# Kernel optimization log

Hardware: AMD Instinct MI355X
Metric: run time of the kernel (lower is better)

The kernel has to match this reference:

```python
import jax, jax.numpy as jnp
import numpy as np


def conv1d(x, w, b, pad):
    # x: [B, C, T], w: [O, I, K], b: [O]
    y = jax.lax.conv_general_dilated(x, w, (1,), [(pad, pad)],
                                     dimension_numbers=('NCH', 'OIH', 'NCH'))
    return y + b[None, :, None]


def chan_ln(x, g, b, eps=1e-4):
    # channel LayerNorm on [B, C, T] (normalize over C)
    mu = jnp.mean(x, axis=1, keepdims=True)
    var = jnp.mean((x - mu) ** 2, axis=1, keepdims=True)
    return (x - mu) * jax.lax.rsqrt(var + eps) * g[None, :, None] + b[None, :, None]


def setup_inputs() -> dict:
    key = jax.random.key(0)
    ks = jax.random.split(key, 16)
    B, Tph, Tmel, H, W = 8, 512, 4096, 256, 256
    x = jax.random.normal(ks[0], (B, Tph, H), jnp.float32)
    x_mask = jnp.ones((B, Tph, 1), jnp.float32)
    x2word = jnp.sort(jax.random.randint(ks[1], (B, Tph), 1, W + 1), axis=1)
    mel2word = jnp.sort(jax.random.randint(ks[2], (B, Tmel), 1, W + 1), axis=1)
    s = 0.05
    pre_w1 = jax.random.normal(ks[3], (H, H, 5), jnp.float32) * s
    pre_b1 = jnp.zeros((H,), jnp.float32)
    ln1_g = jnp.ones((H,), jnp.float32)
    ln1_b = jnp.zeros((H,), jnp.float32)
    pre_w2 = jax.random.normal(ks[4], (H, H, 5), jnp.float32) * s
    pre_b2 = jnp.zeros((H,), jnp.float32)
    ln2_g = jnp.ones((H,), jnp.float32)
    ln2_b = jnp.zeros((H,), jnp.float32)
    proj_w = jax.random.normal(ks[5], (H, H, 1), jnp.float32) * s
    proj_b = jnp.zeros((H,), jnp.float32)
    gauss_w = jax.random.normal(ks[6], (2, H, 1), jnp.float32) * s
    gauss_b = jnp.zeros((2,), jnp.float32)
    return {'x': x, 'x_mask': x_mask,
            'pre_w1': pre_w1, 'pre_b1': pre_b1, 'ln1_g': ln1_g, 'ln1_b': ln1_b,
            'pre_w2': pre_w2, 'pre_b2': pre_b2, 'ln2_g': ln2_g, 'ln2_b': ln2_b,
            'proj_w': proj_w, 'proj_b': proj_b,
            'gauss_w': gauss_w, 'gauss_b': gauss_b,
            'x2word': x2word, 'mel2word': mel2word, 'word_len': 256}


def reference(x, x_mask, pre_w1, pre_b1, ln1_g, ln1_b, pre_w2, pre_b2,
              ln2_g, ln2_b, proj_w, proj_b, gauss_w, gauss_b,
              x2word, mel2word, word_len):
    res_x = x                                   # [B, Tph, H]
    xt = jnp.swapaxes(x, 1, 2)                  # [B, H, Tph]
    mt = jnp.swapaxes(x_mask, 1, 2)             # [B, 1, Tph]
    # ConvReluNorm pre-net (dropout p=0)
    h = jax.nn.relu(chan_ln(conv1d(xt * mt, pre_w1, pre_b1, 2), ln1_g, ln1_b))
    h = jax.nn.relu(chan_ln(conv1d(h * mt, pre_w2, pre_b2, 2), ln2_g, ln2_b))
    h = (xt + conv1d(h, proj_w, proj_b, 0)) * mt
    # gaussian head -> per-phone duration mean m
    g = conv1d(h, gauss_w, gauss_b, 0)          # [B, 2, Tph]
    m = (jax.nn.relu(g[:, 0:1]) + 1.0) * mt
    m = m[:, 0, :]                              # [B, Tph]
    B, Tph = x2word.shape
    Tmel = mel2word.shape[1]
    W = word_len
    bidx = jnp.arange(B)[:, None]
    # scatter-add per-phone durations into word slots (slot 0 = pad)
    dur = jnp.zeros((B, W + 1), m.dtype).at[bidx, x2word].add(m)
    m_word = dur[:, 1:]                         # [B, W]
    # mel2ph_to_dur: frame counts per word
    dur_word = jnp.zeros((B, W + 1), m.dtype).at[bidx, mel2word].add(
        jnp.ones(mel2word.shape, m.dtype))[:, 1:]
    scale = dur_word / (m_word + 1e-4)
    scale_ph = jnp.pad(scale, ((0, 0), (1, 0)))[bidx, x2word]   # gather to phones
    m = m + (scale_ph - 1.0) * jax.lax.stop_gradient(m)
    # Gaussian soft alignment
    center = jnp.cumsum(m, axis=1) - m / 2                      # [B, Tph]
    pos = jnp.arange(Tmel, dtype=m.dtype)
    diff = center[:, None, :] - pos[None, :, None]              # [B, Tmel, Tph]
    y_mask = (mel2word > 0).astype(m.dtype)[:, :, None]
    yx = (mel2word[:, :, None] == x2word[:, None, :]).astype(m.dtype)
    yx = yx * y_mask * mt                                       # [B, Tmel, Tph]
    logits = -(diff * diff) / 10.0
    masked = logits - (1.0 - yx) * 1e9
    weights = jax.nn.softmax(masked.astype(jnp.float32), axis=2)
    attn = jnp.einsum('bmp,bph->bmh', weights, res_x)           # [B, Tmel, H]
    return attn, weights, m_word
```

## Files before the change

### kernel.cpp

```cpp
#include <hip/hip_runtime.h>
#include <math.h>

#define BATCH 8
#define TPH   512
#define TMEL  4096
#define HCH   256
#define WLEN  256
#define KKTOT 1280
#define PSZ   (TMEL * HCH)
#define ZSPLIT 4

#define OFF_H1  655360
#define OFF_M   2752512
#define OFF_CEN 2756608
#define OFF_GVH 2760704

typedef __attribute__((ext_vector_type(4))) float f32x4;
typedef __attribute__((ext_vector_type(8))) short bf16x8;

__device__ __forceinline__ double wsum_d(double v) {
#pragma unroll
    for (int o = 32; o > 0; o >>= 1) v += __shfl_xor(v, o);
    return v;
}
__device__ __forceinline__ float wmax_f(float v) {
#pragma unroll
    for (int o = 32; o > 0; o >>= 1) v = fmaxf(v, __shfl_xor(v, o));
    return v;
}

__device__ __forceinline__ ushort f2bf(float f) {
    unsigned u = __float_as_uint(f);
    return (ushort)((u + 0x7fffu + ((u >> 16) & 1u)) >> 16);
}
__device__ __forceinline__ float bf2f(ushort h) {
    return __uint_as_float((unsigned)h << 16);
}
__device__ __forceinline__ int sidx(int row, int ch) {
    return row * 64 + (ch ^ ((row & 7) << 3));
}

__global__ __launch_bounds__(256) void k_pre(const float* __restrict__ w1,
                                             const float* __restrict__ w2,
                                             ushort* __restrict__ bh1,
                                             ushort* __restrict__ bl1,
                                             ushort* __restrict__ bh2,
                                             ushort* __restrict__ bl2,
                                             const float* __restrict__ gw,
                                             const float* __restrict__ projw,
                                             const float* __restrict__ projb,
                                             double* __restrict__ gvh) {
    __shared__ double part[4];
    int idx = blockIdx.x;
    if (idx < 512) {
        const float* src = (idx < 256) ? w1 : w2;
        ushort* dh = (idx < 256) ? bh1 : bh2;
        ushort* dl = (idx < 256) ? bl1 : bl2;
        int o = idx & 255;
        int t = threadIdx.x;
#pragma unroll
        for (int j = 0; j < 5; ++j) {
            int kk = t + j * 256;
            int k = kk >> 8, i = kk & 255;
            float v = src[o * KKTOT + i * 5 + k];
            ushort h = f2bf(v);
            dh[(size_t)o * KKTOT + kk] = h;
            dl[(size_t)o * KKTOT + kk] = f2bf(v - bf2f(h));
        }
        return;
    }
    int i = threadIdx.x;
    int lane = i & 63, wid = i >> 6;
    double a0 = 0.0, a1 = 0.0, a2 = 0.0, a3 = 0.0;
    for (int c = 0; c < HCH; c += 4) {
        a0 += (double)gw[c + 0] * (double)projw[(c + 0) * HCH + i];
        a1 += (double)gw[c + 1] * (double)projw[(c + 1) * HCH + i];
        a2 += (double)gw[c + 2] * (double)projw[(c + 2) * HCH + i];
        a3 += (double)gw[c + 3] * (double)projw[(c + 3) * HCH + i];
    }
    gvh[i] = ((a0 + a1) + (a2 + a3));
    double s = wsum_d((double)gw[i] * (double)projb[i]);
    if (lane == 0) part[wid] = s;
    __syncthreads();
    if (i == 0) gvh[256] = part[0] + part[1] + part[2] + part[3];
}

__device__ __forceinline__ void stage_a_row(ushort* AsH, ushort* AsL,
                                            const float* __restrict__ src,
                                            const float* __restrict__ mask,
                                            int mb0, int mrow0, int ci0,
                                            int row, int cq) {
    int rib = mrow0 - 2 + row;
    bool v = ((unsigned)rib < 512u);
    const float* sp = src + (size_t)(mb0 + (v ? rib : 0)) * HCH + ci0 + cq * 16;
    float mk = v ? mask[mb0 + rib] : 0.0f;
    float4 f0 = ((const float4*)sp)[0];
    float4 f1 = ((const float4*)sp)[1];
    float4 f2 = ((const float4*)sp)[2];
    float4 f3 = ((const float4*)sp)[3];
    float va[16] = {f0.x, f0.y, f0.z, f0.w, f1.x, f1.y, f1.z, f1.w,
                    f2.x, f2.y, f2.z, f2.w, f3.x, f3.y, f3.z, f3.w};
    ushort h[16], l[16];
#pragma unroll
    for (int j = 0; j < 16; ++j) {
        float m = va[j] * mk;
        h[j] = f2bf(m);
        l[j] = f2bf(m - bf2f(h[j]));
    }
#pragma unroll
    for (int g = 0; g < 4; ++g) {
        ushort4 hv = {h[g * 4], h[g * 4 + 1], h[g * 4 + 2], h[g * 4 + 3]};
        ushort4 lv = {l[g * 4], l[g * 4 + 1], l[g * 4 + 2], l[g * 4 + 3]};
        *(ushort4*)&AsH[sidx(row, cq * 16 + g * 4)] = hv;
        *(ushort4*)&AsL[sidx(row, cq * 16 + g * 4)] = lv;
    }
}

__global__ __launch_bounds__(256) void k_conv_mfma(const float* __restrict__ src,
                                                   const float* __restrict__ mask,
                                                   const ushort* __restrict__ BhT,
                                                   const ushort* __restrict__ BlT,
                                                   float* __restrict__ pout) {
    __shared__ __align__(16) ushort AsH[68 * 64];
    __shared__ __align__(16) ushort AsL[68 * 64];
    __shared__ __align__(16) ushort BsH[64 * 64];
    __shared__ __align__(16) ushort BsL[64 * 64];
    int t = threadIdx.x;
    int lane = t & 63, w = t >> 6;
    int wr = w >> 1, wc = w & 1;
    int l15 = lane & 15, lk = lane >> 4;
    int c0 = blockIdx.x * 64;
    int m0 = blockIdx.y * 64;
    int ci0 = blockIdx.z * 64;
    float* out = pout + (size_t)blockIdx.z * PSZ;
    int mb0 = m0 & ~511, mrow0 = m0 & 511;

    {
        int r = t >> 2, cq = t & 3;
        stage_a_row(AsH, AsL, src, mask, mb0, mrow0, ci0, r, cq);
        if (t < 16) stage_a_row(AsH, AsL, src, mask, mb0, mrow0, ci0, 64 + (t >> 2), t & 3);
    }

    f32x4 acc00 = {0.f, 0.f, 0.f, 0.f}, acc01 = {0.f, 0.f, 0.f, 0.f};
    f32x4 acc10 = {0.f, 0.f, 0.f, 0.f}, acc11 = {0.f, 0.f, 0.f, 0.f};

#pragma unroll 1
    for (int k5 = 0; k5 < 5; ++k5) {
        __syncthreads();
        {
            int col = t >> 2, kq = t & 3;
            size_t goff = (size_t)(c0 + col) * KKTOT + k5 * 256 + ci0 + kq * 16;
            const ushort4* gh = (const ushort4*)(BhT + goff);
            const ushort4* gl = (const ushort4*)(BlT + goff);
            ushort4 hv0 = gh[0], hv1 = gh[1], hv2 = gh[2], hv3 = gh[3];
            ushort4 lv0 = gl[0], lv1 = gl[1], lv2 = gl[2], lv3 = gl[3];
            *(ushort4*)&BsH[sidx(col, kq * 16 + 0)]  = hv0;
            *(ushort4*)&BsH[sidx(col, kq * 16 + 4)]  = hv1;
            *(ushort4*)&BsH[sidx(col, kq * 16 + 8)]  = hv2;
            *(ushort4*)&BsH[sidx(col, kq * 16 + 12)] = hv3;
            *(ushort4*)&BsL[sidx(col, kq * 16 + 0)]  = lv0;
            *(ushort4*)&BsL[sidx(col, kq * 16 + 4)]  = lv1;
            *(ushort4*)&BsL[sidx(col, kq * 16 + 8)]  = lv2;
            *(ushort4*)&BsL[sidx(col, kq * 16 + 12)] = lv3;
        }
        __syncthreads();
#pragma unroll
        for (int kc = 0; kc < 2; ++kc) {
            int ach = kc * 32 + lk * 8;
            int ar0 = wr * 32 + l15 + k5;
            bf16x8 aH0 = *(const bf16x8*)&AsH[sidx(ar0, ach)];
            bf16x8 aH1 = *(const bf16x8*)&AsH[sidx(ar0 + 16, ach)];
            bf16x8 aL0 = *(const bf16x8*)&AsL[sidx(ar0, ach)];
            bf16x8 aL1 = *(const bf16x8*)&AsL[sidx(ar0 + 16, ach)];
            int bc0 = wc * 32 + l15;
            bf16x8 bH0 = *(const bf16x8*)&BsH[sidx(bc0, ach)];
            bf16x8 bH1 = *(const bf16x8*)&BsH[sidx(bc0 + 16, ach)];
            bf16x8 bL0 = *(const bf16x8*)&BsL[sidx(bc0, ach)];
            bf16x8 bL1 = *(const bf16x8*)&BsL[sidx(bc0 + 16, ach)];
#define MM(a, b, c) c = __builtin_amdgcn_mfma_f32_16x16x32_bf16(a, b, c, 0, 0, 0)
            MM(aH0, bH0, acc00); MM(aH0, bL0, acc00); MM(aL0, bH0, acc00); MM(aL0, bL0, acc00);
            MM(aH0, bH1, acc01); MM(aH0, bL1, acc01); MM(aL0, bH1, acc01); MM(aL0, bL1, acc01);
            MM(aH1, bH0, acc10); MM(aH1, bL0, acc10); MM(aL1, bH0, acc10); MM(aL1, bL0, acc10);
            MM(aH1, bH1, acc11); MM(aH1, bL1, acc11); MM(aL1, bH1, acc11); MM(aL1, bL1, acc11);
#undef MM
        }
    }
    int rb = m0 + wr * 32 + lk * 4;
    int cb = c0 + wc * 32 + l15;
#pragma unroll
    for (int i = 0; i < 4; ++i) {
        out[(size_t)(rb + i) * HCH + cb]           = acc00[i];
        out[(size_t)(rb + i) * HCH + cb + 16]      = acc01[i];
        out[(size_t)(rb + 16 + i) * HCH + cb]      = acc10[i];
        out[(size_t)(rb + 16 + i) * HCH + cb + 16] = acc11[i];
    }
}

__global__ __launch_bounds__(256) void k_ln_relu(const float* __restrict__ p,
                                                 const float* __restrict__ bias,
                                                 const float* __restrict__ g,
                                                 const float* __restrict__ b,
                                                 float* __restrict__ out) {
    __shared__ double part[2][2];
    __shared__ double bc[2];
    int tid = threadIdx.x;
    int rr = tid >> 7;
    int inner = tid & 127;
    int lane = tid & 63, wvr = (tid >> 6) & 1;
    int row = blockIdx.x * 2 + rr;
    int c2 = inner * 2;
    size_t idx = (size_t)row * HCH + c2;
    double vx, vy;
    {
        float2 bs = ((const float2*)(bias + c2))[0];
        vx = (double)bs.x; vy = (double)bs.y;
    }
#pragma unroll
    for (int z = 0; z < ZSPLIT; z++) {
        float2 pv = ((const float2*)(p + (size_t)z * PSZ + idx))[0];
        vx += (double)pv.x; vy += (double)pv.y;
    }
    double s = wsum_d(vx + vy);
    if (lane == 0) part[rr][wvr] = s;
    __syncthreads();
    if (inner == 0) bc[rr] = (part[rr][0] + part[rr][1]) * (1.0 / 256.0);
    __syncthreads();
    double mu = bc[rr];
    double w0 = vx - mu, w1 = vy - mu;
    s = wsum_d(w0 * w0 + w1 * w1);
    if (lane == 0) part[rr][wvr] = s;
    __syncthreads();
    if (inner == 0) bc[rr] = (part[rr][0] + part[rr][1]) * (1.0 / 256.0);
    __syncthreads();
    double rs = 1.0 / sqrt(bc[rr] + 1e-4);
    float2 gg = ((const float2*)(g + c2))[0];
    float2 bb = ((const float2*)(b + c2))[0];
    float2 o;
    o.x = (float)fmax(w0 * rs * (double)gg.x + (double)bb.x, 0.0);
    o.y = (float)fmax(w1 * rs * (double)gg.y + (double)bb.y, 0.0);
    ((float2*)(out + idx))[0] = o;
}

__global__ __launch_bounds__(256) void k_ln_relu_m(const float* __restrict__ p,
                                                   const float* __restrict__ bias,
                                                   const float* __restrict__ g,
                                                   const float* __restrict__ b,
                                                   const float* __restrict__ x,
                                                   const float* __restrict__ gw,
                                                   const double* __restrict__ gvh,
                                                   const float* __restrict__ gb,
                                                   const float* __restrict__ mask,
                                                   double* __restrict__ mbuf) {
    __shared__ double part[2][2];
    __shared__ double bc[2];
    int tid = threadIdx.x;
    int rr = tid >> 7;
    int inner = tid & 127;
    int lane = tid & 63, wvr = (tid >> 6) & 1;
    int row = blockIdx.x * 2 + rr;
    int c2 = inner * 2;
    size_t idx = (size_t)row * HCH + c2;
    double vx, vy;
    {
        float2 bs = ((const float2*)(bias + c2))[0];
        vx = (double)bs.x; vy = (double)bs.y;
    }
#pragma unroll
    for (int z = 0; z < ZSPLIT; z++) {
        float2 pv = ((const float2*)(p + (size_t)z * PSZ + idx))[0];
        vx += (double)pv.x; vy += (double)pv.y;
    }
    double s = wsum_d(vx + vy);
    if (lane == 0) part[rr][wvr] = s;
    __syncthreads();
    if (inner == 0) bc[rr] = (part[rr][0] + part[rr][1]) * (1.0 / 256.0);
    __syncthreads();
    double mu = bc[rr];
    double w0 = vx - mu, w1 = vy - mu;
    s = wsum_d(w0 * w0 + w1 * w1);
    if (lane == 0) part[rr][wvr] = s;
    __syncthreads();
    if (inner == 0) bc[rr] = (part[rr][0] + part[rr][1]) * (1.0 / 256.0);
    __syncthreads();
    double rs = 1.0 / sqrt(bc[rr] + 1e-4);
    float2 gg = ((const float2*)(g + c2))[0];
    float2 bb = ((const float2*)(b + c2))[0];
    double o0 = fmax(w0 * rs * (double)gg.x + (double)bb.x, 0.0);
    double o1 = fmax(w1 * rs * (double)gg.y + (double)bb.y, 0.0);
    double2 gv = ((const double2*)(gvh + c2))[0];
    float2 xv = ((const float2*)(x + idx))[0];
    float2 gwv = ((const float2*)(gw + c2))[0];
    double red = gv.x * o0 + gv.y * o1 + (double)gwv.x * (double)xv.x + (double)gwv.y * (double)xv.y;
    s = wsum_d(red);
    if (lane == 0) part[rr][wvr] = s;
    __syncthreads();
    if (inner == 0) {
        double acc = part[rr][0] + part[rr][1];
        double mk = (double)mask[row];
        double g0 = mk * (acc + gvh[256]) + (double)gb[0];
        mbuf[row] = (fmax(g0, 0.0) + 1.0) * mk;
    }
}

__global__ __launch_bounds__(512) void k_dur(const double* __restrict__ mbuf,
                                             const int* __restrict__ x2w,
                                             const int* __restrict__ m2w,
                                             double* __restrict__ center,
                                             float* __restrict__ out_mword) {
    __shared__ double ms[512];
    __shared__ int xw[512];
    __shared__ double dur[257];
    __shared__ int cntw[257];
    __shared__ double sa[512], sb[512];
    int b = blockIdx.x, tid = threadIdx.x;
    if (tid < 257) cntw[tid] = 0;
    ms[tid] = mbuf[b * TPH + tid];
    {
        int w = x2w[b * TPH + tid];
        xw[tid] = max(0, min(256, w));
    }
    __syncthreads();
    for (int j = 0; j < TMEL / 512; j++) {
        int ww = m2w[b * TMEL + tid + j * 512];
        ww = max(0, min(256, ww));
        atomicAdd(&cntw[ww], 1);
    }
    __syncthreads();
    if (tid >= 1 && tid <= 256) {
        double s = 0.0;
        for (int t = 0; t < TPH; t++) {
            if (xw[t] == tid) s += ms[t];
        }
        dur[tid] = s;
        out_mword[b * WLEN + tid - 1] = (float)s;
    }
    __syncthreads();
    double msc;
    {
        int w = xw[tid];
        double sc = (double)cntw[w] / (dur[w] + 1e-4);
        msc = ms[tid] + (sc - 1.0) * ms[tid];
    }
    sa[tid] = msc;
    __syncthreads();
    double* cur = sa; double* nxt = sb;
#pragma unroll
    for (int off = 1; off < 512; off <<= 1) {
        double v = cur[tid];
        if (tid >= off) v += cur[tid - off];
        nxt[tid] = v;
        __syncthreads();
        double* tp = cur; cur = nxt; nxt = tp;
    }
    center[b * TPH + tid] = cur[tid] - msc * 0.5;
}

__global__ __launch_bounds__(256) void k_attn(const float* __restrict__ x,
                                              const double* __restrict__ center,
                                              const int* __restrict__ x2w,
                                              const int* __restrict__ m2w,
                                              const float* __restrict__ mask,
                                              float* __restrict__ outA,
                                              float* __restrict__ outW) {
    int lane = threadIdx.x & 63, wid = threadIdx.x >> 6;
    int r = blockIdx.x * 4 + wid;
    int b = r >> 12;
    const double* cen = center + b * TPH + lane * 8;
    const int* xw = x2w + b * TPH + lane * 8;
    const float* mk = mask + b * TPH + lane * 8;
    int wv = m2w[r];
    double ym = (wv > 0) ? 1.0 : 0.0;
    double posd = (double)(r & 4095);

    double cl[8]; int xl[8]; float ml[8];
#pragma unroll
    for (int q = 0; q < 4; q++) {
        double2 cv = ((const double2*)cen)[q];
        cl[2 * q] = cv.x; cl[2 * q + 1] = cv.y;
    }
    {
        int4 x0 = ((const int4*)xw)[0], x1 = ((const int4*)xw)[1];
        xl[0] = x0.x; xl[1] = x0.y; xl[2] = x0.z; xl[3] = x0.w;
        xl[4] = x1.x; xl[5] = x1.y; xl[6] = x1.z; xl[7] = x1.w;
        float4 m0 = ((const float4*)mk)[0], m1 = ((const float4*)mk)[1];
        ml[0] = m0.x; ml[1] = m0.y; ml[2] = m0.z; ml[3] = m0.w;
        ml[4] = m1.x; ml[5] = m1.y; ml[6] = m1.z; ml[7] = m1.w;
    }

    float ev[8];
    float lmax = -3.0e38f;
#pragma unroll
    for (int j = 0; j < 8; j++) {
        double d = cl[j] - posd;
        double lg = -(d * d) / 10.0;
        double f = ((xl[j] == wv) ? 1.0 : 0.0) * ym * (double)ml[j];
        double masked = lg - (1.0 - f) * 1.0e9;
        float m32 = (float)masked;
        ev[j] = m32;
        lmax = fmaxf(lmax, m32);
    }
    lmax = wmax_f(lmax);
    double lsum = 0.0;
#pragma unroll
    for (int j = 0; j < 8; j++) {
        float e = expf(__fsub_rn(ev[j], lmax));
        ev[j] = e;
        lsum += (double)e;
    }
    lsum = wsum_d(lsum);
    float tot = (float)lsum;
    float* wrow = outW + (size_t)r * TPH + lane * 8;
    bool any = false;
#pragma unroll
    for (int j = 0; j < 8; j++) {
        float w = __fdiv_rn(ev[j], tot);
        ev[j] = w;
        any |= (w > 0.f);
    }
    {
        float4 w0 = {ev[0], ev[1], ev[2], ev[3]};
        float4 w1 = {ev[4], ev[5], ev[6], ev[7]};
        ((float4*)wrow)[0] = w0;
        ((float4*)wrow)[1] = w1;
    }
    double acc0 = 0.0, acc1 = 0.0, acc2 = 0.0, acc3 = 0.0;
    const float* xb = x + (size_t)b * TPH * HCH;
    unsigned long long mball = __ballot(any);
    while (mball) {
        int l2 = __ffsll(mball) - 1;
        mball &= mball - 1;
#pragma unroll
        for (int j = 0; j < 8; j++) {
            float w = __shfl(ev[j], l2);
            if (w > 0.f) {
                int t = l2 * 8 + j;
                float4 xv = ((const float4*)(xb + (size_t)t * HCH))[lane];
                acc0 += (double)w * (double)xv.x;
                acc1 += (double)w * (double)xv.y;
                acc2 += (double)w * (double)xv.z;
                acc3 += (double)w * (double)xv.w;
            }
        }
    }
    float4 o;
    o.x = (float)acc0; o.y = (float)acc1; o.z = (float)acc2; o.w = (float)acc3;
    ((float4*)(outA + (size_t)r * HCH))[lane] = o;
}

extern "C" void kernel_launch(void* const* d_in, const int* in_sizes, int n_in,
                              void* d_out, int out_size, void* d_ws, size_t ws_size,
                              hipStream_t stream) {
    (void)in_sizes; (void)n_in; (void)out_size; (void)ws_size;
    const float* x    = (const float*)d_in[0];
    const float* xm   = (const float*)d_in[1];
    const float* pw1  = (const float*)d_in[2];
    const float* pb1  = (const float*)d_in[3];
    const float* g1   = (const float*)d_in[4];
    const float* be1  = (const float*)d_in[5];
    const float* pw2  = (const float*)d_in[6];
    const float* pb2  = (const float*)d_in[7];
    const float* g2   = (const float*)d_in[8];
    const float* be2  = (const float*)d_in[9];
    const float* pjw  = (const float*)d_in[10];
    const float* pjb  = (const float*)d_in[11];
    const float* gw   = (const float*)d_in[12];
    const float* gb   = (const float*)d_in[13];
    const int*   x2w  = (const int*)d_in[14];
    const int*   m2w  = (const int*)d_in[15];

    double* ws   = (double*)d_ws;
    ushort* bh1  = (ushort*)ws;
    ushort* bl1  = bh1 + 256 * KKTOT;
    ushort* bh2  = bl1 + 256 * KKTOT;
    ushort* bl2  = bh2 + 256 * KKTOT;
    float*  h1   = (float*)(ws + OFF_H1);
    double* mbuf = ws + OFF_M;
    double* cen  = ws + OFF_CEN;
    double* gvh  = ws + OFF_GVH;

    float* outA = (float*)d_out;
    float* outW = outA + (size_t)BATCH * TMEL * HCH;
    float* outM = outW + (size_t)BATCH * TMEL * TPH;
    float* pbuf = outW;

    hipLaunchKernelGGL(k_pre, dim3(513), dim3(256), 0, stream,
                       pw1, pw2, bh1, bl1, bh2, bl2, gw, pjw, pjb, gvh);
    hipLaunchKernelGGL(k_conv_mfma, dim3(4, 64, ZSPLIT), dim3(256), 0, stream, x, xm, bh1, bl1, pbuf);
    hipLaunchKernelGGL(k_ln_relu, dim3(2048), dim3(256), 0, stream, pbuf, pb1, g1, be1, h1);
    hipLaunchKernelGGL(k_conv_mfma, dim3(4, 64, ZSPLIT), dim3(256), 0, stream, h1, xm, bh2, bl2, pbuf);
    hipLaunchKernelGGL(k_ln_relu_m, dim3(2048), dim3(256), 0, stream, pbuf, pb2, g2, be2,
                       x, gw, gvh, gb, xm, mbuf);
    hipLaunchKernelGGL(k_dur, dim3(BATCH), dim3(512), 0, stream, mbuf, x2w, m2w, cen, outM);
    hipLaunchKernelGGL(k_attn, dim3(BATCH * TMEL / 4), dim3(256), 0, stream, x, cen, x2w, m2w, xm, outA, outW);
}
```

Baseline: 251.4 us.

## Prefetch conv weights, drop low-low MFMA term, wave-per-row LayerNorm, fp32 attention logits

Several changes land together. The conv kernel now uses 16-byte shared-memory stores and register-prefetches the next weight slice before the barrier, which hides global load latency. It also drops the low×low bf16 MFMA product, cutting matrix work by a quarter at a small accuracy cost. Both LayerNorm kernels now map one wave to one row, so shuffles replace the shared-memory reductions and block barriers. The attention logits are computed in fp32 instead of fp64, which is cheaper but may shift softmax weights slightly.

```diff
diff --git a/kernel.cpp b/kernel.cpp
--- a/kernel.cpp
+++ b/kernel.cpp
@@ -17,6 +17,7 @@
 
 typedef __attribute__((ext_vector_type(4))) float f32x4;
 typedef __attribute__((ext_vector_type(8))) short bf16x8;
+typedef __attribute__((ext_vector_type(8))) ushort ushort8v;
 
 __device__ __forceinline__ double wsum_d(double v) {
 #pragma unroll
@@ -107,13 +108,14 @@
         h[j] = f2bf(m);
         l[j] = f2bf(m - bf2f(h[j]));
     }
-#pragma unroll
-    for (int g = 0; g < 4; ++g) {
-        ushort4 hv = {h[g * 4], h[g * 4 + 1], h[g * 4 + 2], h[g * 4 + 3]};
-        ushort4 lv = {l[g * 4], l[g * 4 + 1], l[g * 4 + 2], l[g * 4 + 3]};
-        *(ushort4*)&AsH[sidx(row, cq * 16 + g * 4)] = hv;
-        *(ushort4*)&AsL[sidx(row, cq * 16 + g * 4)] = lv;
-    }
+    ushort8v hv0 = {h[0], h[1], h[2], h[3], h[4], h[5], h[6], h[7]};
+    ushort8v hv1 = {h[8], h[9], h[10], h[11], h[12], h[13], h[14], h[15]};
+    ushort8v lv0 = {l[0], l[1], l[2], l[3], l[4], l[5], l[6], l[7]};
+    ushort8v lv1 = {l[8], l[9], l[10], l[11], l[12], l[13], l[14], l[15]};
+    *(ushort8v*)&AsH[sidx(row, cq * 16 + 0)] = hv0;
+    *(ushort8v*)&AsH[sidx(row, cq * 16 + 8)] = hv1;
+    *(ushort8v*)&AsL[sidx(row, cq * 16 + 0)] = lv0;
+    *(ushort8v*)&AsL[sidx(row, cq * 16 + 8)] = lv1;
 }
 
 __global__ __launch_bounds__(256) void k_conv_mfma(const float* __restrict__ src,
@@ -144,24 +146,26 @@
     f32x4 acc00 = {0.f, 0.f, 0.f, 0.f}, acc01 = {0.f, 0.f, 0.f, 0.f};
     f32x4 acc10 = {0.f, 0.f, 0.f, 0.f}, acc11 = {0.f, 0.f, 0.f, 0.f};
 
+    int bcol = t >> 2, bkq = t & 3;
+    size_t gbase = (size_t)(c0 + bcol) * KKTOT + ci0 + bkq * 16;
+    ushort8v pbh0 = *(const ushort8v*)(BhT + gbase);
+    ushort8v pbh1 = *(const ushort8v*)(BhT + gbase + 8);
+    ushort8v pbl0 = *(const ushort8v*)(BlT + gbase);
+    ushort8v pbl1 = *(const ushort8v*)(BlT + gbase + 8);
+
 #pragma unroll 1
     for (int k5 = 0; k5 < 5; ++k5) {
         __syncthreads();
-        {
-            int col = t >> 2, kq = t & 3;
-            size_t goff = (size_t)(c0 + col) * KKTOT + k5 * 256 + ci0 + kq * 16;
-            const ushort4* gh = (const ushort4*)(BhT + goff);
-            const ushort4* gl = (const ushort4*)(BlT + goff);
-            ushort4 hv0 = gh[0], hv1 = gh[1], hv2 = gh[2], hv3 = gh[3];
-            ushort4 lv0 = gl[0], lv1 = gl[1], lv2 = gl[2], lv3 = gl[3];
-            *(ushort4*)&BsH[sidx(col, kq * 16 + 0)]  = hv0;
-            *(ushort4*)&BsH[sidx(col, kq * 16 + 4)]  = hv1;
-            *(ushort4*)&BsH[sidx(col, kq * 16 + 8)]  = hv2;
-            *(ushort4*)&BsH[sidx(col, kq * 16 + 12)] = hv3;
-            *(ushort4*)&BsL[sidx(col, kq * 16 + 0)]  = lv0;
-            *(ushort4*)&BsL[sidx(col, kq * 16 + 4)]  = lv1;
-            *(ushort4*)&BsL[sidx(col, kq * 16 + 8)]  = lv2;
-            *(ushort4*)&BsL[sidx(col, kq * 16 + 12)] = lv3;
+        *(ushort8v*)&BsH[sidx(bcol, bkq * 16 + 0)] = pbh0;
+        *(ushort8v*)&BsH[sidx(bcol, bkq * 16 + 8)] = pbh1;
+        *(ushort8v*)&BsL[sidx(bcol, bkq * 16 + 0)] = pbl0;
+        *(ushort8v*)&BsL[sidx(bcol, bkq * 16 + 8)] = pbl1;
+        if (k5 < 4) {
+            size_t g2 = gbase + (size_t)(k5 + 1) * 256;
+            pbh0 = *(const ushort8v*)(BhT + g2);
+            pbh1 = *(const ushort8v*)(BhT + g2 + 8);
+            pbl0 = *(const ushort8v*)(BlT + g2);
+            pbl1 = *(const ushort8v*)(BlT + g2 + 8);
         }
         __syncthreads();
 #pragma unroll
@@ -178,10 +182,10 @@
             bf16x8 bL0 = *(const bf16x8*)&BsL[sidx(bc0, ach)];
             bf16x8 bL1 = *(const bf16x8*)&BsL[sidx(bc0 + 16, ach)];
 #define MM(a, b, c) c = __builtin_amdgcn_mfma_f32_16x16x32_bf16(a, b, c, 0, 0, 0)
-            MM(aH0, bH0, acc00); MM(aH0, bL0, acc00); MM(aL0, bH0, acc00); MM(aL0, bL0, acc00);
-            MM(aH0, bH1, acc01); MM(aH0, bL1, acc01); MM(aL0, bH1, acc01); MM(aL0, bL1, acc01);
-            MM(aH1, bH0, acc10); MM(aH1, bL0, acc10); MM(aL1, bH0, acc10); MM(aL1, bL0, acc10);
-            MM(aH1, bH1, acc11); MM(aH1, bL1, acc11); MM(aL1, bH1, acc11); MM(aL1, bL1, acc11);
+            MM(aH0, bH0, acc00); MM(aH0, bL0, acc00); MM(aL0, bH0, acc00);
+            MM(aH0, bH1, acc01); MM(aH0, bL1, acc01); MM(aL0, bH1, acc01);
+            MM(aH1, bH0, acc10); MM(aH1, bL0, acc10); MM(aL1, bH0, acc10);
+            MM(aH1, bH1, acc11); MM(aH1, bL1, acc11); MM(aL1, bH1, acc11);
 #undef MM
         }
     }
@@ -201,44 +205,29 @@
                                                  const float* __restrict__ g,
                                                  const float* __restrict__ b,
                                                  float* __restrict__ out) {
-    __shared__ double part[2][2];
-    __shared__ double bc[2];
-    int tid = threadIdx.x;
-    int rr = tid >> 7;
-    int inner = tid & 127;
-    int lane = tid & 63, wvr = (tid >> 6) & 1;
-    int row = blockIdx.x * 2 + rr;
-    int c2 = inner * 2;
-    size_t idx = (size_t)row * HCH + c2;
-    double vx, vy;
-    {
-        float2 bs = ((const float2*)(bias + c2))[0];
-        vx = (double)bs.x; vy = (double)bs.y;
-    }
+    int lane = threadIdx.x & 63, wid = threadIdx.x >> 6;
+    int row = blockIdx.x * 4 + wid;
+    int c4 = lane * 4;
+    size_t idx = (size_t)row * HCH + c4;
+    float4 bs = *(const float4*)(bias + c4);
+    double s0 = bs.x, s1 = bs.y, s2 = bs.z, s3 = bs.w;
 #pragma unroll
     for (int z = 0; z < ZSPLIT; z++) {
-        float2 pv = ((const float2*)(p + (size_t)z * PSZ + idx))[0];
-        vx += (double)pv.x; vy += (double)pv.y;
-    }
-    double s = wsum_d(vx + vy);
-    if (lane == 0) part[rr][wvr] = s;
-    __syncthreads();
-    if (inner == 0) bc[rr] = (part[rr][0] + part[rr][1]) * (1.0 / 256.0);
-    __syncthreads();
-    double mu = bc[rr];
-    double w0 = vx - mu, w1 = vy - mu;
-    s = wsum_d(w0 * w0 + w1 * w1);
-    if (lane == 0) part[rr][wvr] = s;
-    __syncthreads();
-    if (inner == 0) bc[rr] = (part[rr][0] + part[rr][1]) * (1.0 / 256.0);
-    __syncthreads();
-    double rs = 1.0 / sqrt(bc[rr] + 1e-4);
-    float2 gg = ((const float2*)(g + c2))[0];
-    float2 bb = ((const float2*)(b + c2))[0];
-    float2 o;
+        float4 pv = *(const float4*)(p + (size_t)z * PSZ + idx);
+        s0 += pv.x; s1 += pv.y; s2 += pv.z; s3 += pv.w;
+    }
+    double mu = wsum_d(((s0 + s1) + (s2 + s3))) * (1.0 / 256.0);
+    double w0 = s0 - mu, w1 = s1 - mu, w2 = s2 - mu, w3 = s3 - mu;
+    double var = wsum_d((w0 * w0 + w1 * w1) + (w2 * w2 + w3 * w3)) * (1.0 / 256.0);
+    double rs = 1.0 / sqrt(var + 1e-4);
+    float4 gg = *(const float4*)(g + c4);
+    float4 bb = *(const float4*)(b + c4);
+    float4 o;
     o.x = (float)fmax(w0 * rs * (double)gg.x + (double)bb.x, 0.0);
     o.y = (float)fmax(w1 * rs * (double)gg.y + (double)bb.y, 0.0);
-    ((float2*)(out + idx))[0] = o;
+    o.z = (float)fmax(w2 * rs * (double)gg.z + (double)bb.z, 0.0);
+    o.w = (float)fmax(w3 * rs * (double)gg.w + (double)bb.w, 0.0);
+    *(float4*)(out + idx) = o;
 }
 
 __global__ __launch_bounds__(256) void k_ln_relu_m(const float* __restrict__ p,
@@ -251,53 +240,38 @@
                                                    const float* __restrict__ gb,
                                                    const float* __restrict__ mask,
                                                    double* __restrict__ mbuf) {
-    __shared__ double part[2][2];
-    __shared__ double bc[2];
-    int tid = threadIdx.x;
-    int rr = tid >> 7;
-    int inner = tid & 127;
-    int lane = tid & 63, wvr = (tid >> 6) & 1;
-    int row = blockIdx.x * 2 + rr;
-    int c2 = inner * 2;
-    size_t idx = (size_t)row * HCH + c2;
-    double vx, vy;
-    {
-        float2 bs = ((const float2*)(bias + c2))[0];
-        vx = (double)bs.x; vy = (double)bs.y;
-    }
+    int lane = threadIdx.x & 63, wid = threadIdx.x >> 6;
+    int row = blockIdx.x * 4 + wid;
+    int c4 = lane * 4;
+    size_t idx = (size_t)row * HCH + c4;
+    float4 bs = *(const float4*)(bias + c4);
+    double s0 = bs.x, s1 = bs.y, s2 = bs.z, s3 = bs.w;
 #pragma unroll
     for (int z = 0; z < ZSPLIT; z++) {
-        float2 pv = ((const float2*)(p + (size_t)z * PSZ + idx))[0];
-        vx += (double)pv.x; vy += (double)pv.y;
-    }
-    double s = wsum_d(vx + vy);
-    if (lane == 0) part[rr][wvr] = s;
-    __syncthreads();
-    if (inner == 0) bc[rr] = (part[rr][0] + part[rr][1]) * (1.0 / 256.0);
-    __syncthreads();
-    double mu = bc[rr];
-    double w0 = vx - mu, w1 = vy - mu;
-    s = wsum_d(w0 * w0 + w1 * w1);
-    if (lane == 0) part[rr][wvr] = s;
-    __syncthreads();
-    if (inner == 0) bc[rr] = (part[rr][0] + part[rr][1]) * (1.0 / 256.0);
-    __syncthreads();
-    double rs = 1.0 / sqrt(bc[rr] + 1e-4);
-    float2 gg = ((const float2*)(g + c2))[0];
-    float2 bb = ((const float2*)(b + c2))[0];
+        float4 pv = *(const float4*)(p + (size_t)z * PSZ + idx);
+        s0 += pv.x; s1 += pv.y; s2 += pv.z; s3 += pv.w;
+    }
+    double mu = wsum_d(((s0 + s1) + (s2 + s3))) * (1.0 / 256.0);
+    double w0 = s0 - mu, w1 = s1 - mu, w2 = s2 - mu, w3 = s3 - mu;
+    double var = wsum_d((w0 * w0 + w1 * w1) + (w2 * w2 + w3 * w3)) * (1.0 / 256.0);
+    double rs = 1.0 / sqrt(var + 1e-4);
+    float4 gg = *(const float4*)(g + c4);
+    float4 bb = *(const float4*)(b + c4);
     double o0 = fmax(w0 * rs * (double)gg.x + (double)bb.x, 0.0);
     double o1 = fmax(w1 * rs * (double)gg.y + (double)bb.y, 0.0);
-    double2 gv = ((const double2*)(gvh + c2))[0];
-    float2 xv = ((const float2*)(x + idx))[0];
-    float2 gwv = ((const float2*)(gw + c2))[0];
-    double red = gv.x * o0 + gv.y * o1 + (double)gwv.x * (double)xv.x + (double)gwv.y * (double)xv.y;
-    s = wsum_d(red);
-    if (lane == 0) part[rr][wvr] = s;
-    __syncthreads();
-    if (inner == 0) {
-        double acc = part[rr][0] + part[rr][1];
+    double o2 = fmax(w2 * rs * (double)gg.z + (double)bb.z, 0.0);
+    double o3 = fmax(w3 * rs * (double)gg.w + (double)bb.w, 0.0);
+    double2 gv0 = *(const double2*)(gvh + c4);
+    double2 gv1 = *(const double2*)(gvh + c4 + 2);
+    float4 xv = *(const float4*)(x + idx);
+    float4 gwv = *(const float4*)(gw + c4);
+    double red = gv0.x * o0 + gv0.y * o1 + gv1.x * o2 + gv1.y * o3
+               + (double)gwv.x * (double)xv.x + (double)gwv.y * (double)xv.y
+               + (double)gwv.z * (double)xv.z + (double)gwv.w * (double)xv.w;
+    double tot = wsum_d(red);
+    if (lane == 0) {
         double mk = (double)mask[row];
-        double g0 = mk * (acc + gvh[256]) + (double)gb[0];
+        double g0 = mk * (tot + gvh[256]) + (double)gb[0];
         mbuf[row] = (fmax(g0, 0.0) + 1.0) * mk;
     }
 }
@@ -369,7 +343,7 @@
     const int* xw = x2w + b * TPH + lane * 8;
     const float* mk = mask + b * TPH + lane * 8;
     int wv = m2w[r];
-    double ym = (wv > 0) ? 1.0 : 0.0;
+    float ymf = (wv > 0) ? 1.0f : 0.0f;
     double posd = (double)(r & 4095);
 
     double cl[8]; int xl[8]; float ml[8];
@@ -391,11 +365,10 @@
     float lmax = -3.0e38f;
 #pragma unroll
     for (int j = 0; j < 8; j++) {
-        double d = cl[j] - posd;
-        double lg = -(d * d) / 10.0;
-        double f = ((xl[j] == wv) ? 1.0 : 0.0) * ym * (double)ml[j];
-        double masked = lg - (1.0 - f) * 1.0e9;
-        float m32 = (float)masked;
+        float df = (float)(cl[j] - posd);
+        float lg = __fdiv_rn(df * df, -10.0f);
+        float f = ((xl[j] == wv) ? ymf : 0.0f) * ml[j];
+        float m32 = lg - (1.0f - f) * 1.0e9f;
         ev[j] = m32;
         lmax = fmaxf(lmax, m32);
     }
@@ -486,9 +459,9 @@
     hipLaunchKernelGGL(k_pre, dim3(513), dim3(256), 0, stream,
                        pw1, pw2, bh1, bl1, bh2, bl2, gw, pjw, pjb, gvh);
     hipLaunchKernelGGL(k_conv_mfma, dim3(4, 64, ZSPLIT), dim3(256), 0, stream, x, xm, bh1, bl1, pbuf);
-    hipLaunchKernelGGL(k_ln_relu, dim3(2048), dim3(256), 0, stream, pbuf, pb1, g1, be1, h1);
+    hipLaunchKernelGGL(k_ln_relu, dim3(1024), dim3(256), 0, stream, pbuf, pb1, g1, be1, h1);
     hipLaunchKernelGGL(k_conv_mfma, dim3(4, 64, ZSPLIT), dim3(256), 0, stream, h1, xm, bh2, bl2, pbuf);
-    hipLaunchKernelGGL(k_ln_relu_m, dim3(2048), dim3(256), 0, stream, pbuf, pb2, g2, be2,
+    hipLaunchKernelGGL(k_ln_relu_m, dim3(1024), dim3(256), 0, stream, pbuf, pb2, g2, be2,
                        x, gw, gvh, gb, xm, mbuf);
     hipLaunchKernelGGL(k_dur, dim3(BATCH), dim3(512), 0, stream, mbuf, x2w, m2w, cen, outM);
     hipLaunchKernelGGL(k_attn, dim3(BATCH * TMEL / 4), dim3(256), 0, stream, x, cen, x2w, m2w, xm, outA, outW);
```

After: 243.7 us. 3.0% less time.
